# Performance work log

Measured on AMD Instinct MI355X. Metric: run time of the kernel, lower is better.

Reference implementation:

```python
import jax, jax.numpy as jnp
import numpy as np

IOU_THRESHOLD = 0.5  # default iou_threshold of nms/class_spec_nms


def _nms_keep_mask(boxes, scores, iou_threshold):
    """Faithful port of the hand-rolled greedy NMS.

    The torch version builds a variable-length index list; here we return the
    equivalent fixed-shape boolean keep mask over the N boxes (jit-friendly).
    """
    n = scores.shape[0]
    x1, y1, x2, y2 = boxes[:, 0], boxes[:, 1], boxes[:, 2], boxes[:, 3]
    areas = (x2 - x1) * (y2 - y1)                       # [N]
    # pairwise intersection via broadcasted min/max (same math as the matmul-
    # with-ones trick in the source, without materializing the ones matrices)
    xi = jnp.minimum(x2[:, None], x2[None, :]) - jnp.maximum(x1[:, None], x1[None, :])
    yi = jnp.minimum(y2[:, None], y2[None, :]) - jnp.maximum(y1[:, None], y1[None, :])
    inter = jnp.maximum(xi, 0.0) * jnp.maximum(yi, 0.0)  # [N,N]
    iou = inter / (areas[:, None] + areas[None, :] - inter)

    first_max = scores.max()
    first_min = scores.min()
    curr_idx0 = jnp.argmax(scores)

    # carry: (candidate mask, working scores copy, keep mask, curr max, curr idx)
    init = (scores < first_max, scores, jnp.zeros((n,), dtype=bool), first_max, curr_idx0)

    def cond(state):
        mask, _, _, cmax, _ = state
        return jnp.any(mask) & (cmax >= first_min)

    def body(state):
        mask, sc, keep, cmax, cidx = state
        mask = mask & (iou[cidx] <= iou_threshold)   # suppress overlaps with current max
        mask = mask.at[cidx].set(False)
        keep = keep.at[cidx].set(True)               # keep current max
        sc = jnp.where(mask, sc, first_min - 1.0)    # kill suppressed scores
        cidx = jnp.argmax(sc)
        return mask, sc, keep, sc[cidx], cidx

    _, _, keep, _, _ = jax.lax.while_loop(cond, body, init)
    return keep


def setup_inputs() -> dict:
    key = jax.random.key(0)
    k1, k2, k3, k4, k5, k6 = jax.random.split(key, 6)
    N = 4096    # pre-NMS candidate boxes
    L = 16384   # p3 locations for a 1024x1024 image at stride 8 (128*128)
    xy = jax.random.uniform(k1, (N, 2), dtype=jnp.float32) * 900.0
    wh = jax.random.uniform(k2, (N, 2), dtype=jnp.float32) * 100.0 + 1.0
    boxes = jnp.concatenate([xy, xy + wh], axis=1)          # valid x1<x2, y1<y2
    scores = jax.random.uniform(k3, (N,), dtype=jnp.float32)
    class_ids = jax.random.randint(k4, (N,), 0, 80, dtype=jnp.int32)
    locations = jax.random.uniform(k5, (L, 2), dtype=jnp.float32) * 1024.0
    deltas = jax.random.uniform(k6, (L, 4), dtype=jnp.float32)  # positive gt deltas
    return {"boxes": boxes, "scores": scores, "class_ids": class_ids,
            "locations": locations, "deltas": deltas, "stride": 8}


def reference(boxes, scores, class_ids, locations, deltas, stride):
    # ---- class_spec_nms: class-offset trick then plain NMS ----
    max_coordinate = boxes.max()
    offsets = class_ids.astype(boxes.dtype) * (max_coordinate + 1.0)
    boxes_for_nms = boxes + offsets[:, None]
    keep_mask = _nms_keep_mask(boxes_for_nms, scores, IOU_THRESHOLD)

    # ---- fcos_apply_deltas_to_locations ----
    clipped = jnp.maximum(deltas, 0.0)
    s = jnp.asarray(stride, dtype=deltas.dtype)
    px, py = locations[:, 0], locations[:, 1]
    pred_boxes = jnp.stack([px - clipped[:, 0] * s,
                            py - clipped[:, 1] * s,
                            px + clipped[:, 2] * s,
                            py + clipped[:, 3] * s], axis=1)  # [L,4]

    # ---- fcos_make_centerness_targets ----
    lr_min = jnp.minimum(deltas[:, 0], deltas[:, 2])
    tb_min = jnp.minimum(deltas[:, 1], deltas[:, 3])
    lr_max = jnp.maximum(deltas[:, 0], deltas[:, 2])
    tb_max = jnp.maximum(deltas[:, 1], deltas[:, 3])
    centerness = jnp.sqrt((lr_min * tb_min) / (lr_max * tb_max))
    centerness = jnp.where(jnp.all(deltas == -1.0, axis=1), -1.0, centerness)

    pred_out = jnp.concatenate([pred_boxes, centerness[:, None]], axis=1)  # [L,5]
    return keep_mask, pred_out
```

## Files before the change

kernel.cpp:

```cpp
#include <hip/hip_runtime.h>
#include <stdint.h>

#define NB 4096
#define NBLK 64
#define IOU_THR 0.5f
#define ECAP 1024
#define RANKB 256
#define NTRI (NBLK * (NBLK + 1) / 2)

typedef unsigned long long u64;

__device__ __forceinline__ u64 readlane64(u64 v, int lane) {
    unsigned lo = (unsigned)__builtin_amdgcn_readlane((int)(unsigned)(v & 0xffffffffull), lane);
    unsigned hi = (unsigned)__builtin_amdgcn_readlane((int)(unsigned)(v >> 32), lane);
    return ((u64)hi << 32) | (u64)lo;
}

__global__ void __launch_bounds__(256) fused_front(
        const float* __restrict__ boxes, const float* __restrict__ scores,
        const int* __restrict__ cls,
        const float* __restrict__ loc, const float* __restrict__ deltas,
        const int* __restrict__ stride_p,
        float* __restrict__ pred_out, int* __restrict__ sidx,
        float* __restrict__ sboxes, float* __restrict__ sareas,
        int* __restrict__ counts ) {
    __shared__ __align__(16) float sh[NB];
    __shared__ float red[4];
    int blk = blockIdx.x;
    int t = threadIdx.x;

    if (blk < 64) {
        int i = blk * 256 + t;
        float s = (float)stride_p[0];
        float2 p = ((const float2*)loc)[i];
        float4 d = ((const float4*)deltas)[i];
        float c0 = fmaxf(d.x, 0.f), c1 = fmaxf(d.y, 0.f);
        float c2 = fmaxf(d.z, 0.f), c3 = fmaxf(d.w, 0.f);
        float b0 = p.x - c0 * s;
        float b1 = p.y - c1 * s;
        float b2 = p.x + c2 * s;
        float b3 = p.y + c3 * s;
        float lr_min = fminf(d.x, d.z), tb_min = fminf(d.y, d.w);
        float lr_max = fmaxf(d.x, d.z), tb_max = fmaxf(d.y, d.w);
        float cent = sqrtf((lr_min * tb_min) / (lr_max * tb_max));
        if (d.x == -1.f && d.y == -1.f && d.z == -1.f && d.w == -1.f) cent = -1.f;
        float* o = pred_out + (size_t)i * 5;
        o[0] = b0; o[1] = b1; o[2] = b2; o[3] = b3; o[4] = cent;
    } else if (blk < 64 + RANKB) {
        for (int i = t; i < NB; i += 256) sh[i] = scores[i];
        float m = -3.0e38f;
        for (int i = t; i < NB * 4; i += 256) m = fmaxf(m, boxes[i]);
        for (int o = 32; o > 0; o >>= 1) m = fmaxf(m, __shfl_down(m, o));
        if ((t & 63) == 0) red[t >> 6] = m;
        __syncthreads();
        float mc1 = fmaxf(fmaxf(red[0], red[1]), fmaxf(red[2], red[3])) + 1.0f;

        int wave = t >> 6, lane = t & 63;
        int base = (blk - 64) * 16 + wave * 4;
        float my0 = sh[base + 0], my1 = sh[base + 1];
        float my2 = sh[base + 2], my3 = sh[base + 3];
        int c0 = 0, c1 = 0, c2 = 0, c3 = 0;
#pragma unroll 8
        for (int k = 0; k < 64; ++k) {
            int j = lane + k * 64;
            float sj = sh[j];
            c0 += (sj > my0) || (sj == my0 && j < base + 0);
            c1 += (sj > my1) || (sj == my1 && j < base + 1);
            c2 += (sj > my2) || (sj == my2 && j < base + 2);
            c3 += (sj > my3) || (sj == my3 && j < base + 3);
        }
        for (int o = 32; o > 0; o >>= 1) {
            c0 += __shfl_down(c0, o); c1 += __shfl_down(c1, o);
            c2 += __shfl_down(c2, o); c3 += __shfl_down(c3, o);
        }
        if (lane == 0) {
            int rk[4] = { c0, c1, c2, c3 };
#pragma unroll
            for (int k = 0; k < 4; ++k) {
                int i = base + k, rank = rk[k];
                sidx[rank] = i;
                float off = (float)cls[i] * mc1;
                float4 b = ((const float4*)boxes)[i];
                b.x += off; b.y += off; b.z += off; b.w += off;
                ((float4*)sboxes)[rank] = b;
                sareas[rank] = (b.z - b.x) * (b.w - b.y);
            }
        }
    } else {
        if (t < 2 * NBLK + 1) counts[t] = 0;
    }
}

__global__ void __launch_bounds__(64) edge_kernel(
        const float* __restrict__ sboxes, const float* __restrict__ sareas,
        const int* __restrict__ sidx,
        int* __restrict__ counts ,
        uint4* __restrict__ entries, float* __restrict__ keep_out) {
    int idx = blockIdx.x, r = 0;
    while (idx >= NBLK - r) { idx -= NBLK - r; ++r; }
    int c = r + idx;

    __shared__ float4 cb[64];
    __shared__ float ca[64];
    __shared__ int islast;
    int t = threadIdx.x;

    float4 rb = ((const float4*)sboxes)[r * 64 + t];
    float ra = sareas[r * 64 + t];
    if (c == r) {
        cb[t] = rb; ca[t] = ra;
    } else {
        cb[t] = ((const float4*)sboxes)[c * 64 + t];
        ca[t] = sareas[c * 64 + t];
    }
    __syncthreads();

    u64 w = 0;
#pragma unroll 8
    for (int j = 0; j < 64; ++j) {
        float4 b = cb[j];
        float xi = fminf(rb.z, b.z) - fmaxf(rb.x, b.x);
        float yi = fminf(rb.w, b.w) - fmaxf(rb.y, b.y);
        float inter = fmaxf(xi, 0.f) * fmaxf(yi, 0.f);
        float iou = inter / (ra + ca[j] - inter);
        w |= (u64)(iou > IOU_THR) << j;
    }
    if (c == r) w &= ~(1ull << t);
    if (w) {
        int slot = atomicAdd(&counts[r], 1);
        if (slot < ECAP) {
            u64* e = (u64*)&entries[r * ECAP + slot];
            atomicExch(e,     (u64)(unsigned)(t | (c << 8)));
            atomicExch(e + 1, w);
        }
    }

    asm volatile("s_waitcnt vmcnt(0)" ::: "memory");
    if (t == 0) {
        islast = 0;
        int old = atomicAdd(&counts[NBLK + r], 1);
        if (old == (NBLK - r) - 1) {
            int o2 = atomicAdd(&counts[2 * NBLK], 1);
            islast = (o2 == NBLK - 1);
        }
    }
    __syncthreads();
    if (!islast) return;
    __threadfence();

    const int lane = t;
    int cnt_l = counts[lane];
    u64 accv = 0;
    u64 keptall = 0;
    u64 self = 1ull << lane;

    uint4 cur = entries[lane];
    uint4 n1  = entries[ECAP + lane];
    for (int b = 0; b < NBLK; ++b) {
        uint4 n2;
        if (b < NBLK - 2) n2 = entries[(u64)(b + 2) * ECAP + lane];

        int cnt = __builtin_amdgcn_readlane(cnt_l, b);
        if (cnt > ECAP) cnt = ECAP;
        int cfast = cnt < 64 ? cnt : 64;

        u64 colw = self;
        for (int e = 0; e < cfast; ++e) {
            unsigned meta = (unsigned)__builtin_amdgcn_readlane((int)cur.x, e);
            int l = meta & 255, cw = meta >> 8;
            if (cw == b) {
                unsigned lo = (unsigned)__builtin_amdgcn_readlane((int)cur.z, e);
                unsigned hi = (unsigned)__builtin_amdgcn_readlane((int)cur.w, e);
                if (lane == l) colw |= ((u64)hi << 32) | lo;
            }
        }
        for (int e = 64; e < cnt; ++e) {
            uint4 x = entries[(u64)b * ECAP + e];
            int l = x.x & 255, cw = x.x >> 8;
            if (cw == b && lane == l) colw |= ((u64)x.w << 32) | x.z;
        }

        u64 rem = readlane64(accv, b);
        u64 avail = ~rem;
        u64 edges = colw & avail & ~self;
        u64 involved = __ballot(edges != 0ull) & avail;
        u64 keptm = avail & ~involved;
        u64 sub = involved;
        while (sub) {
            int i = (int)__builtin_ctzll(sub);
            keptm |= 1ull << i;
            u64 ci = readlane64(colw, i);
            sub &= ~(ci | (1ull << i));
        }
        if (lane == b) keptall = keptm;

        for (int e = 0; e < cfast; ++e) {
            unsigned meta = (unsigned)__builtin_amdgcn_readlane((int)cur.x, e);
            unsigned lo   = (unsigned)__builtin_amdgcn_readlane((int)cur.z, e);
            unsigned hi   = (unsigned)__builtin_amdgcn_readlane((int)cur.w, e);
            int l = meta & 255, cw = meta >> 8;
            if (((keptm >> l) & 1ull) && lane == cw) accv |= ((u64)hi << 32) | lo;
        }
        for (int e = 64; e < cnt; ++e) {
            uint4 x = entries[(u64)b * ECAP + e];
            int l = x.x & 255, cw = x.x >> 8;
            if (((keptm >> l) & 1ull) && lane == cw) accv |= ((u64)x.w << 32) | x.z;
        }
        cur = n1; n1 = n2;
    }

#pragma unroll 8
    for (int bb = 0; bb < NBLK; ++bb) {
        u64 kw = readlane64(keptall, bb);
        int oidx = sidx[bb * 64 + lane];
        keep_out[oidx] = ((kw >> lane) & 1ull) ? 1.0f : 0.0f;
    }
}

extern "C" void kernel_launch(void* const* d_in, const int* in_sizes, int n_in,
                              void* d_out, int out_size, void* d_ws, size_t ws_size,
                              hipStream_t stream) {
    const float* boxes   = (const float*)d_in[0];
    const float* scores  = (const float*)d_in[1];
    const int*   cls     = (const int*)d_in[2];
    const float* loc     = (const float*)d_in[3];
    const float* deltas  = (const float*)d_in[4];
    const int*   stride  = (const int*)d_in[5];

    float* out = (float*)d_out;
    float* keep_out = out;
    float* pred_out = out + NB;

    char* ws = (char*)d_ws;
    int*   sidx    = (int*)ws;                       ws += NB * sizeof(int);
    float* sboxes  = (float*)ws;                     ws += NB * 4 * sizeof(float);
    float* sareas  = (float*)ws;                     ws += NB * sizeof(float);
    int*   counts  = (int*)ws;                       ws += (2 * NBLK + 1) * sizeof(int) + 12;
    uint4* entries = (uint4*)ws;

    fused_front<<<64 + RANKB + 1, 256, 0, stream>>>(boxes, scores, cls, loc, deltas,
                                                    stride, pred_out, sidx, sboxes,
                                                    sareas, counts);
    edge_kernel<<<NTRI, 64, 0, stream>>>(sboxes, sareas, sidx, counts, entries,
                                         keep_out);
}
```

Before: 128.4 us.

## Compute max coordinate once and scatter edges via LDS atomics

The global box-coordinate max reduction, which every rank block used to recompute, now runs once in the spare block and is stored in workspace. Edge blocks read it, then apply the class offset and compute areas themselves. In the final sequential NMS sweep, two serial 64-iteration readlane loops are replaced by parallel LDS atomicOr scatters with barriers. This shortens the serial critical path but adds shared-memory atomics and syncs on every block iteration.

```diff
diff --git a/kernel.cpp b/kernel.cpp
--- a/kernel.cpp
+++ b/kernel.cpp
@@ -22,7 +22,8 @@
         const float* __restrict__ loc, const float* __restrict__ deltas,
         const int* __restrict__ stride_p,
         float* __restrict__ pred_out, int* __restrict__ sidx,
-        float* __restrict__ sboxes, float* __restrict__ sareas,
+        float* __restrict__ sboxes, int* __restrict__ scls,
+        float* __restrict__ maxc,
         int* __restrict__ counts ) {
     __shared__ __align__(16) float sh[NB];
     __shared__ float red[4];
@@ -48,13 +49,7 @@
         o[0] = b0; o[1] = b1; o[2] = b2; o[3] = b3; o[4] = cent;
     } else if (blk < 64 + RANKB) {
         for (int i = t; i < NB; i += 256) sh[i] = scores[i];
-        float m = -3.0e38f;
-        for (int i = t; i < NB * 4; i += 256) m = fmaxf(m, boxes[i]);
-        for (int o = 32; o > 0; o >>= 1) m = fmaxf(m, __shfl_down(m, o));
-        if ((t & 63) == 0) red[t >> 6] = m;
-        __syncthreads();
-        float mc1 = fmaxf(fmaxf(red[0], red[1]), fmaxf(red[2], red[3])) + 1.0f;
-
+        __syncthreads();
         int wave = t >> 6, lane = t & 63;
         int base = (blk - 64) * 16 + wave * 4;
         float my0 = sh[base + 0], my1 = sh[base + 1];
@@ -79,21 +74,24 @@
             for (int k = 0; k < 4; ++k) {
                 int i = base + k, rank = rk[k];
                 sidx[rank] = i;
-                float off = (float)cls[i] * mc1;
-                float4 b = ((const float4*)boxes)[i];
-                b.x += off; b.y += off; b.z += off; b.w += off;
-                ((float4*)sboxes)[rank] = b;
-                sareas[rank] = (b.z - b.x) * (b.w - b.y);
+                ((float4*)sboxes)[rank] = ((const float4*)boxes)[i];
+                scls[rank] = cls[i];
             }
         }
     } else {
         if (t < 2 * NBLK + 1) counts[t] = 0;
+        float m = -3.0e38f;
+        for (int i = t; i < NB * 4; i += 256) m = fmaxf(m, boxes[i]);
+        for (int o = 32; o > 0; o >>= 1) m = fmaxf(m, __shfl_down(m, o));
+        if ((t & 63) == 0) red[t >> 6] = m;
+        __syncthreads();
+        if (t == 0) *maxc = fmaxf(fmaxf(red[0], red[1]), fmaxf(red[2], red[3]));
     }
 }
 
 __global__ void __launch_bounds__(64) edge_kernel(
-        const float* __restrict__ sboxes, const float* __restrict__ sareas,
-        const int* __restrict__ sidx,
+        const float* __restrict__ sboxes, const int* __restrict__ scls,
+        const int* __restrict__ sidx, const float* __restrict__ maxc,
         int* __restrict__ counts ,
         uint4* __restrict__ entries, float* __restrict__ keep_out) {
     int idx = blockIdx.x, r = 0;
@@ -102,16 +100,23 @@
 
     __shared__ float4 cb[64];
     __shared__ float ca[64];
+    __shared__ u64 lw[64];
     __shared__ int islast;
     int t = threadIdx.x;
+    float mc1 = maxc[0] + 1.0f;
 
     float4 rb = ((const float4*)sboxes)[r * 64 + t];
-    float ra = sareas[r * 64 + t];
+    float offr = (float)scls[r * 64 + t] * mc1;
+    rb.x += offr; rb.y += offr; rb.z += offr; rb.w += offr;
+    float ra = (rb.z - rb.x) * (rb.w - rb.y);
+
     if (c == r) {
         cb[t] = rb; ca[t] = ra;
     } else {
-        cb[t] = ((const float4*)sboxes)[c * 64 + t];
-        ca[t] = sareas[c * 64 + t];
+        float4 b = ((const float4*)sboxes)[c * 64 + t];
+        float offc = (float)scls[c * 64 + t] * mc1;
+        b.x += offc; b.y += offc; b.z += offc; b.w += offc;
+        cb[t] = b; ca[t] = (b.z - b.x) * (b.w - b.y);
     }
     __syncthreads();
 
@@ -164,19 +169,19 @@
         if (cnt > ECAP) cnt = ECAP;
         int cfast = cnt < 64 ? cnt : 64;
 
-        u64 colw = self;
-        for (int e = 0; e < cfast; ++e) {
-            unsigned meta = (unsigned)__builtin_amdgcn_readlane((int)cur.x, e);
-            int l = meta & 255, cw = meta >> 8;
-            if (cw == b) {
-                unsigned lo = (unsigned)__builtin_amdgcn_readlane((int)cur.z, e);
-                unsigned hi = (unsigned)__builtin_amdgcn_readlane((int)cur.w, e);
-                if (lane == l) colw |= ((u64)hi << 32) | lo;
-            }
-        }
+        bool mine = lane < cfast;
+        int  el = (int)(cur.x & 255u);
+        int  ec = (int)((cur.x >> 8) & 255u);
+        u64  ew = ((u64)cur.w << 32) | cur.z;
+
+        lw[lane] = 0;
+        __syncthreads();
+        if (mine && ec == b) atomicOr(&lw[el & 63], ew);
+        __syncthreads();
+        u64 colw = lw[lane] | self;
         for (int e = 64; e < cnt; ++e) {
             uint4 x = entries[(u64)b * ECAP + e];
-            int l = x.x & 255, cw = x.x >> 8;
+            int l = x.x & 255, cw = (x.x >> 8) & 255;
             if (cw == b && lane == l) colw |= ((u64)x.w << 32) | x.z;
         }
 
@@ -194,16 +199,14 @@
         }
         if (lane == b) keptall = keptm;
 
-        for (int e = 0; e < cfast; ++e) {
-            unsigned meta = (unsigned)__builtin_amdgcn_readlane((int)cur.x, e);
-            unsigned lo   = (unsigned)__builtin_amdgcn_readlane((int)cur.z, e);
-            unsigned hi   = (unsigned)__builtin_amdgcn_readlane((int)cur.w, e);
-            int l = meta & 255, cw = meta >> 8;
-            if (((keptm >> l) & 1ull) && lane == cw) accv |= ((u64)hi << 32) | lo;
-        }
+        lw[lane] = 0;
+        __syncthreads();
+        if (mine && ((keptm >> el) & 1ull)) atomicOr(&lw[ec & 63], ew);
+        __syncthreads();
+        accv |= lw[lane];
         for (int e = 64; e < cnt; ++e) {
             uint4 x = entries[(u64)b * ECAP + e];
-            int l = x.x & 255, cw = x.x >> 8;
+            int l = x.x & 255, cw = (x.x >> 8) & 255;
             if (((keptm >> l) & 1ull) && lane == cw) accv |= ((u64)x.w << 32) | x.z;
         }
         cur = n1; n1 = n2;
@@ -232,15 +235,16 @@
     float* pred_out = out + NB;
 
     char* ws = (char*)d_ws;
+    float* maxc    = (float*)ws;                     ws += 16;
     int*   sidx    = (int*)ws;                       ws += NB * sizeof(int);
     float* sboxes  = (float*)ws;                     ws += NB * 4 * sizeof(float);
-    float* sareas  = (float*)ws;                     ws += NB * sizeof(float);
+    int*   scls    = (int*)ws;                       ws += NB * sizeof(int);
     int*   counts  = (int*)ws;                       ws += (2 * NBLK + 1) * sizeof(int) + 12;
     uint4* entries = (uint4*)ws;
 
     fused_front<<<64 + RANKB + 1, 256, 0, stream>>>(boxes, scores, cls, loc, deltas,
                                                     stride, pred_out, sidx, sboxes,
-                                                    sareas, counts);
-    edge_kernel<<<NTRI, 64, 0, stream>>>(sboxes, sareas, sidx, counts, entries,
+                                                    scls, maxc, counts);
+    edge_kernel<<<NTRI, 64, 0, stream>>>(sboxes, scls, sidx, maxc, counts, entries,
                                          keep_out);
 }
```

Result: faster. 119.2 us (-7.2%).
